# Kernel tuning notes

Hardware: AMD Instinct MI355X
Metric: run time of the kernel (lower is better)

The kernel has to match this reference:

```python
import jax, jax.numpy as jnp
import numpy as np

N_DRUGS = 4096
W_DIM = 512
N_SUB = 10
N_EDGES = 131072


def setup_inputs() -> dict:
    key = jax.random.key(0)
    k1, k2, k3, k4 = jax.random.split(key, 4)
    z_drug = jax.random.normal(k1, (N_DRUGS, W_DIM), dtype=jnp.float32)
    # glorot-ish init for weights
    global_weight = jax.random.normal(k2, (W_DIM, W_DIM), dtype=jnp.float32) * (2.0 / (2 * W_DIM)) ** 0.5
    local_diag = jax.random.normal(k3, (N_SUB, W_DIM), dtype=jnp.float32) * (2.0 / (W_DIM + 1)) ** 0.5
    batch_edges = jax.random.randint(k4, (2, N_EDGES), 0, N_DRUGS, dtype=jnp.int64)
    return {
        "z_drug": z_drug,
        "global_weight": global_weight,
        "local_diag": local_diag,
        "batch_edges": batch_edges,
        "edge_sub_type_idx": 2,
    }


def reference(z_drug, global_weight, local_diag, batch_edges, edge_sub_type_idx):
    # edge_type == 'drug_drug': z1 = z2 = z_drug
    row_embed = z_drug[batch_edges[0]]            # [B, D]
    col_embed = z_drug[batch_edges[1]]            # [B, D]
    d = local_diag[edge_sub_type_idx]             # [D] diagonal of local weight matrix
    # row @ diag(d) @ W @ diag(d) == ((row * d) @ W) * d
    p = ((row_embed * d) @ global_weight) * d     # [B, D]
    # diagonal(p @ col^T) == rowwise dot product
    score = jnp.sum(p * col_embed, axis=-1)       # [B]
    return jax.nn.sigmoid(score)
```

## Files before the change

kernel.cpp:

```cpp
#include <hip/hip_runtime.h>
#include <cstdint>

#define ND 4096
#define D  512

typedef __bf16 bf16x8 __attribute__((ext_vector_type(8)));
typedef float floatx4 __attribute__((ext_vector_type(4)));
typedef unsigned short ushort8 __attribute__((ext_vector_type(8)));

__device__ __forceinline__ float bf2f(unsigned short b) {
    return __uint_as_float(((unsigned int)b) << 16);
}
__device__ __forceinline__ unsigned short f2bf(float f) {
    unsigned int u = __float_as_uint(f);
    u += 0x7fffu + ((u >> 16) & 1u);
    return (unsigned short)(u >> 16);
}
__device__ __forceinline__ float lo16(unsigned int u) { return __uint_as_float(u << 16); }
__device__ __forceinline__ float hi16(unsigned int u) { return __uint_as_float(u & 0xffff0000u); }

__device__ __forceinline__ void gll16(const void* g, void* l) {
    __builtin_amdgcn_global_load_lds((const __attribute__((address_space(1))) unsigned int*)g,
                                     (__attribute__((address_space(3))) unsigned int*)l,
                                     16, 0, 0);
}

union U8B8 { ushort8 u; bf16x8 b; };

__device__ __forceinline__ int2 detect_flags(const unsigned short* z, const int* ed) {
    int lane = threadIdx.x & 63;
    unsigned short u = z[lane];
    int e = (u >> 7) & 0xFF;
    unsigned long long b0 = __ballot(e >= 96 && e <= 160);
    unsigned long long b1 = __ballot(ed[2 * lane + 1] == 0);
    int2 f;
    f.x = (__popcll(b0) >= 56) ? 1 : 0;
    f.y = (__popcll(b1) >= 56) ? 1 : 0;
    return f;
}

__global__ __launch_bounds__(256) void prep_kernel(const void* __restrict__ Wv,
                                                   const void* __restrict__ ldv,
                                                   const int* __restrict__ sub,
                                                   unsigned short* __restrict__ Mt,
                                                   unsigned short* __restrict__ zb,
                                                   const void* __restrict__ z,
                                                   const int* __restrict__ ed) {
    __shared__ float xp[64][65];
    int2 f = detect_flags((const unsigned short*)z, ed);
    int bf = f.x;

    if (blockIdx.x >= 64) {
        if (bf) return;
        int idx = (int)(blockIdx.x - 64) * 256 + threadIdx.x;
        const float* zf = (const float*)z;
#pragma unroll
        for (int it = 0; it < 4; it++) {
            int base = (it * 65536 + idx) * 8;
            float4 f0 = *(const float4*)(zf + base);
            float4 f1 = *(const float4*)(zf + base + 4);
            union { ushort8 u; uint4 v; } cv;
            cv.u[0] = f2bf(f0.x); cv.u[1] = f2bf(f0.y);
            cv.u[2] = f2bf(f0.z); cv.u[3] = f2bf(f0.w);
            cv.u[4] = f2bf(f1.x); cv.u[5] = f2bf(f1.y);
            cv.u[6] = f2bf(f1.z); cv.u[7] = f2bf(f1.w);
            *(uint4*)(zb + base) = cv.v;
        }
        return;
    }

    int su = sub[0];
    if ((unsigned)su > 9u) su = 2;
    int k0 = (blockIdx.x & 7) * 64, n0 = (blockIdx.x >> 3) * 64;
    int j = threadIdx.x & 63, w = threadIdx.x >> 6;
#pragma unroll
    for (int r = 0; r < 16; r++) {
        int k = k0 + w * 16 + r;
        float v = bf ? bf2f(((const unsigned short*)Wv)[k * D + n0 + j])
                     : ((const float*)Wv)[k * D + n0 + j];
        xp[w * 16 + r][j] = v;
    }
    __syncthreads();
    int k = k0 + j;
    float dk = bf ? bf2f(((const unsigned short*)ldv)[su * D + k])
                  : ((const float*)ldv)[su * D + k];
#pragma unroll
    for (int r = 0; r < 16; r++) {
        int n = n0 + w * 16 + r;
        float dn = bf ? bf2f(((const unsigned short*)ldv)[su * D + n])
                      : ((const float*)ldv)[su * D + n];
        Mt[n * D + k] = f2bf(xp[j][w * 16 + r] * dk * dn);
    }
}

__global__ __launch_bounds__(256) void gemm_kernel(const void* __restrict__ z,
                                                   const unsigned short* __restrict__ zb,
                                                   const unsigned short* __restrict__ Mt,
                                                   unsigned short* __restrict__ Y,
                                                   const int* __restrict__ ed) {
    __shared__ __bf16 As[2][8 * 512];
    __shared__ __bf16 Bs[2][8 * 512];
    int2 f = detect_flags((const unsigned short*)z, ed);
    const unsigned short* A = f.x ? (const unsigned short*)z : zb;

    int tid = threadIdx.x;
    int w = tid >> 6, lane = tid & 63;
    int rl = lane & 15, quad = lane >> 4;
    int bx = blockIdx.x;
    int xcd = bx & 7, idx = bx >> 3;
    int tm = (xcd * 8 + (idx & 7)) * 64;
    int tn = (idx >> 3) * 64;
    int wm = (w >> 1) * 32, wn = (w & 1) * 32;

    const unsigned short* Ap = A + (tm + lane) * D;
    const unsigned short* Bp = Mt + (tn + lane) * D;

    floatx4 acc[2][2] = {};

    auto stage = [&](int buf, int kk) {
#pragma unroll
        for (int t = 0; t < 2; t++) {
            int kb = w * 2 + t;
            gll16(Bp + kk + kb * 8, &Bs[buf][kb * 512]);
            gll16(Ap + kk + kb * 8, &As[buf][kb * 512]);
        }
    };
    auto compute = [&](int buf) {
#pragma unroll
        for (int kc = 0; kc < 64; kc += 32) {
            int kb0 = kc >> 3;
            bf16x8 a0 = *(const bf16x8*)(&As[buf][(kb0 + quad) * 512 + (wm + rl) * 8]);
            bf16x8 a1 = *(const bf16x8*)(&As[buf][(kb0 + quad) * 512 + (wm + 16 + rl) * 8]);
            bf16x8 b0 = *(const bf16x8*)(&Bs[buf][(kb0 + quad) * 512 + (wn + rl) * 8]);
            bf16x8 b1 = *(const bf16x8*)(&Bs[buf][(kb0 + quad) * 512 + (wn + 16 + rl) * 8]);
            acc[0][0] = __builtin_amdgcn_mfma_f32_16x16x32_bf16(a0, b0, acc[0][0], 0, 0, 0);
            acc[0][1] = __builtin_amdgcn_mfma_f32_16x16x32_bf16(a0, b1, acc[0][1], 0, 0, 0);
            acc[1][0] = __builtin_amdgcn_mfma_f32_16x16x32_bf16(a1, b0, acc[1][0], 0, 0, 0);
            acc[1][1] = __builtin_amdgcn_mfma_f32_16x16x32_bf16(a1, b1, acc[1][1], 0, 0, 0);
        }
    };

    stage(0, 0);
    __syncthreads();
#pragma unroll
    for (int kt = 1; kt < 8; kt++) {
        int cur = (kt - 1) & 1;
        stage(cur ^ 1, kt * 64);
        compute(cur);
        __syncthreads();
    }
    compute(1);

#pragma unroll
    for (int j = 0; j < 2; j++) {
        int col = tn + wn + j * 16 + rl;
#pragma unroll
        for (int i = 0; i < 2; i++) {
            int rbase = tm + wm + i * 16 + quad * 4;
#pragma unroll
            for (int r = 0; r < 4; r++)
                Y[(rbase + r) * D + col] = f2bf(acc[i][j][r]);
        }
    }
}

template <bool BF, bool I64>
__device__ void edge_slice_body(const unsigned short* __restrict__ Y,
                                const void* __restrict__ z,
                                const int* __restrict__ ed,
                                float* __restrict__ partial, int E) {
    int slice = blockIdx.x & 7;
    int egrp  = blockIdx.x >> 3;
    int lane = threadIdx.x & 63;
    int w = threadIdx.x >> 6;
    int sub8 = lane >> 3;
    int l = lane & 7;
    int col = slice * 64 + l * 8;
    int e0 = egrp * 256 + w * 8 + sub8;

    if (egrp * 256 + 255 < E) {
        int r[8], c[8];
#pragma unroll
        for (int i = 0; i < 8; i++) {
            int e = e0 + i * 32;
            if constexpr (I64) { r[i] = ed[2 * e] & (ND - 1); c[i] = ed[2 * (E + e)] & (ND - 1); }
            else               { r[i] = ed[e] & (ND - 1);     c[i] = ed[E + e] & (ND - 1); }
        }
        float s[8];
#pragma unroll
        for (int i = 0; i < 8; i++) {
            uint4 yu = *(const uint4*)(Y + r[i] * D + col);
            if constexpr (BF) {
                uint4 zu = *(const uint4*)((const unsigned short*)z + c[i] * D + col);
                s[i]  = lo16(yu.x) * lo16(zu.x) + hi16(yu.x) * hi16(zu.x);
                s[i] += lo16(yu.y) * lo16(zu.y) + hi16(yu.y) * hi16(zu.y);
                s[i] += lo16(yu.z) * lo16(zu.z) + hi16(yu.z) * hi16(zu.z);
                s[i] += lo16(yu.w) * lo16(zu.w) + hi16(yu.w) * hi16(zu.w);
            } else {
                const float* zf = (const float*)z + c[i] * D + col;
                float4 f0 = *(const float4*)zf;
                float4 f1 = *(const float4*)(zf + 4);
                s[i]  = lo16(yu.x) * f0.x + hi16(yu.x) * f0.y;
                s[i] += lo16(yu.y) * f0.z + hi16(yu.y) * f0.w;
                s[i] += lo16(yu.z) * f1.x + hi16(yu.z) * f1.y;
                s[i] += lo16(yu.w) * f1.z + hi16(yu.w) * f1.w;
            }
        }
#pragma unroll
        for (int i = 0; i < 8; i++) {
            s[i] += __shfl_xor(s[i], 1, 64);
            s[i] += __shfl_xor(s[i], 2, 64);
            s[i] += __shfl_xor(s[i], 4, 64);
            if (l == 0)
                partial[slice * E + e0 + i * 32] = s[i];
        }
    } else {
#pragma unroll
        for (int i = 0; i < 8; i++) {
            int e = e0 + i * 32;
            if (e >= E) continue;
            int r, c;
            if constexpr (I64) { r = ed[2 * e]; c = ed[2 * (E + e)]; }
            else               { r = ed[e];     c = ed[E + e]; }
            r &= ND - 1; c &= ND - 1;
            uint4 yu = *(const uint4*)(Y + r * D + col);
            float s;
            if constexpr (BF) {
                uint4 zu = *(const uint4*)((const unsigned short*)z + c * D + col);
                s  = lo16(yu.x) * lo16(zu.x) + hi16(yu.x) * hi16(zu.x);
                s += lo16(yu.y) * lo16(zu.y) + hi16(yu.y) * hi16(zu.y);
                s += lo16(yu.z) * lo16(zu.z) + hi16(yu.z) * hi16(zu.z);
                s += lo16(yu.w) * lo16(zu.w) + hi16(yu.w) * hi16(zu.w);
            } else {
                const float* zf = (const float*)z + c * D + col;
                float4 f0 = *(const float4*)zf;
                float4 f1 = *(const float4*)(zf + 4);
                s  = lo16(yu.x) * f0.x + hi16(yu.x) * f0.y;
                s += lo16(yu.y) * f0.z + hi16(yu.y) * f0.w;
                s += lo16(yu.z) * f1.x + hi16(yu.z) * f1.y;
                s += lo16(yu.w) * f1.z + hi16(yu.w) * f1.w;
            }
            s += __shfl_xor(s, 1, 64);
            s += __shfl_xor(s, 2, 64);
            s += __shfl_xor(s, 4, 64);
            if (l == 0)
                partial[slice * E + e] = s;
        }
    }
}

__global__ __launch_bounds__(256) void edge_slice(const unsigned short* __restrict__ Y,
                                                  const void* __restrict__ z,
                                                  const int* __restrict__ ed,
                                                  float* __restrict__ partial, int E) {
    int2 f = detect_flags((const unsigned short*)z, ed);
    if (f.x) { if (f.y) edge_slice_body<true, true >(Y, z, ed, partial, E);
               else     edge_slice_body<true, false>(Y, z, ed, partial, E); }
    else     { if (f.y) edge_slice_body<false, true >(Y, z, ed, partial, E);
               else     edge_slice_body<false, false>(Y, z, ed, partial, E); }
}

__global__ __launch_bounds__(256) void finish_kernel(const float* __restrict__ partial,
                                                     const unsigned short* __restrict__ zdet,
                                                     const int* __restrict__ eddet,
                                                     void* __restrict__ out, int E) {
    int2 f = detect_flags(zdet, eddet);
    int e = blockIdx.x * 256 + threadIdx.x;
    if (e >= E) return;
    float t = 0.f;
#pragma unroll
    for (int s = 0; s < 8; s++)
        t += partial[s * E + e];
    if (!(t > -1e30f && t < 1e30f)) t = 0.0f;
    float sig = 1.0f / (1.0f + __expf(-t));
    if (f.x) ((unsigned short*)out)[e] = f2bf(sig);
    else     ((float*)out)[e] = sig;
}

extern "C" void kernel_launch(void* const* d_in, const int* in_sizes, int n_in,
                              void* d_out, int out_size, void* d_ws, size_t ws_size,
                              hipStream_t stream) {
    const void* z     = d_in[0];
    const void* W     = d_in[1];
    const void* ldiag = d_in[2];
    const int* edges  = (const int*)d_in[3];
    const int* sub    = (const int*)d_in[4];
    int E = out_size;

    char* ws = (char*)d_ws;
    unsigned short* Y  = (unsigned short*)ws;
    unsigned short* Mt = (unsigned short*)(ws + 4194304);
    float* partial     = (float*)(ws + 4194304 + 524288);
    unsigned short* zb = (unsigned short*)(ws + 4194304 + 524288 + 4194304);

    prep_kernel<<<320, 256, 0, stream>>>(W, ldiag, sub, Mt, zb, z, edges);
    gemm_kernel<<<512, 256, 0, stream>>>(z, zb, Mt, Y, edges);
    int sblocks = ((E + 255) / 256) * 8;
    edge_slice<<<sblocks, 256, 0, stream>>>(Y, z, edges, partial, E);
    finish_kernel<<<(E + 255) / 256, 256, 0, stream>>>(partial, (const unsigned short*)z,
                                                       edges, d_out, E);
}
```

Before: 107.2 us.

## Fuse four kernels into one cooperative persistent kernel with grid syncs

```diff
diff --git a/kernel.cpp b/kernel.cpp
--- a/kernel.cpp
+++ b/kernel.cpp
@@ -1,5 +1,8 @@
 #include <hip/hip_runtime.h>
+#include <hip/hip_cooperative_groups.h>
 #include <cstdint>
+
+namespace cg = cooperative_groups;
 
 #define ND 4096
 #define D  512
@@ -24,8 +27,6 @@
                                      (__attribute__((address_space(3))) unsigned int*)l,
                                      16, 0, 0);
 }
-
-union U8B8 { ushort8 u; bf16x8 b; };
 
 __device__ __forceinline__ int2 detect_flags(const unsigned short* z, const int* ed) {
     int lane = threadIdx.x & 63;
@@ -39,40 +40,16 @@
     return f;
 }
 
-__global__ __launch_bounds__(256) void prep_kernel(const void* __restrict__ Wv,
-                                                   const void* __restrict__ ldv,
-                                                   const int* __restrict__ sub,
-                                                   unsigned short* __restrict__ Mt,
-                                                   unsigned short* __restrict__ zb,
-                                                   const void* __restrict__ z,
-                                                   const int* __restrict__ ed) {
-    __shared__ float xp[64][65];
-    int2 f = detect_flags((const unsigned short*)z, ed);
-    int bf = f.x;
-
-    if (blockIdx.x >= 64) {
-        if (bf) return;
-        int idx = (int)(blockIdx.x - 64) * 256 + threadIdx.x;
-        const float* zf = (const float*)z;
-#pragma unroll
-        for (int it = 0; it < 4; it++) {
-            int base = (it * 65536 + idx) * 8;
-            float4 f0 = *(const float4*)(zf + base);
-            float4 f1 = *(const float4*)(zf + base + 4);
-            union { ushort8 u; uint4 v; } cv;
-            cv.u[0] = f2bf(f0.x); cv.u[1] = f2bf(f0.y);
-            cv.u[2] = f2bf(f0.z); cv.u[3] = f2bf(f0.w);
-            cv.u[4] = f2bf(f1.x); cv.u[5] = f2bf(f1.y);
-            cv.u[6] = f2bf(f1.z); cv.u[7] = f2bf(f1.w);
-            *(uint4*)(zb + base) = cv.v;
-        }
-        return;
-    }
-
+
+__device__ __forceinline__ void mt_body(const void* __restrict__ Wv,
+                                        const void* __restrict__ ldv,
+                                        const int* __restrict__ sub,
+                                        unsigned short* __restrict__ Mt,
+                                        int bf, int bid, int tid, float (*xp)[65]) {
     int su = sub[0];
     if ((unsigned)su > 9u) su = 2;
-    int k0 = (blockIdx.x & 7) * 64, n0 = (blockIdx.x >> 3) * 64;
-    int j = threadIdx.x & 63, w = threadIdx.x >> 6;
+    int k0 = (bid & 7) * 64, n0 = (bid >> 3) * 64;
+    int j = tid & 63, w = tid >> 6;
 #pragma unroll
     for (int r = 0; r < 16; r++) {
         int k = k0 + w * 16 + r;
@@ -93,46 +70,52 @@
     }
 }
 
-__global__ __launch_bounds__(256) void gemm_kernel(const void* __restrict__ z,
-                                                   const unsigned short* __restrict__ zb,
-                                                   const unsigned short* __restrict__ Mt,
-                                                   unsigned short* __restrict__ Y,
-                                                   const int* __restrict__ ed) {
-    __shared__ __bf16 As[2][8 * 512];
-    __shared__ __bf16 Bs[2][8 * 512];
-    int2 f = detect_flags((const unsigned short*)z, ed);
-    const unsigned short* A = f.x ? (const unsigned short*)z : zb;
-
-    int tid = threadIdx.x;
+__device__ __forceinline__ void zconv_body(const float* __restrict__ zf,
+                                           unsigned short* __restrict__ zb,
+                                           int v0, int stride) {
+    for (int v = v0; v < (ND * D) / 8; v += stride) {
+        int base = v * 8;
+        float4 f0 = *(const float4*)(zf + base);
+        float4 f1 = *(const float4*)(zf + base + 4);
+        union { ushort8 u; uint4 q; } cv;
+        cv.u[0] = f2bf(f0.x); cv.u[1] = f2bf(f0.y);
+        cv.u[2] = f2bf(f0.z); cv.u[3] = f2bf(f0.w);
+        cv.u[4] = f2bf(f1.x); cv.u[5] = f2bf(f1.y);
+        cv.u[6] = f2bf(f1.z); cv.u[7] = f2bf(f1.w);
+        *(uint4*)(zb + base) = cv.q;
+    }
+}
+
+__device__ __forceinline__ void gemm_tile(const unsigned short* __restrict__ A,
+                                          const unsigned short* __restrict__ Mt,
+                                          unsigned short* __restrict__ Y,
+                                          __bf16* As, __bf16* Bs, int bid, int tid) {
     int w = tid >> 6, lane = tid & 63;
     int rl = lane & 15, quad = lane >> 4;
-    int bx = blockIdx.x;
-    int xcd = bx & 7, idx = bx >> 3;
+    int xcd = bid & 7, idx = bid >> 3;
     int tm = (xcd * 8 + (idx & 7)) * 64;
     int tn = (idx >> 3) * 64;
     int wm = (w >> 1) * 32, wn = (w & 1) * 32;
-
     const unsigned short* Ap = A + (tm + lane) * D;
     const unsigned short* Bp = Mt + (tn + lane) * D;
 
     floatx4 acc[2][2] = {};
-
     auto stage = [&](int buf, int kk) {
 #pragma unroll
         for (int t = 0; t < 2; t++) {
             int kb = w * 2 + t;
-            gll16(Bp + kk + kb * 8, &Bs[buf][kb * 512]);
-            gll16(Ap + kk + kb * 8, &As[buf][kb * 512]);
+            gll16(Bp + kk + kb * 8, Bs + buf * 4096 + kb * 512);
+            gll16(Ap + kk + kb * 8, As + buf * 4096 + kb * 512);
         }
     };
     auto compute = [&](int buf) {
 #pragma unroll
         for (int kc = 0; kc < 64; kc += 32) {
             int kb0 = kc >> 3;
-            bf16x8 a0 = *(const bf16x8*)(&As[buf][(kb0 + quad) * 512 + (wm + rl) * 8]);
-            bf16x8 a1 = *(const bf16x8*)(&As[buf][(kb0 + quad) * 512 + (wm + 16 + rl) * 8]);
-            bf16x8 b0 = *(const bf16x8*)(&Bs[buf][(kb0 + quad) * 512 + (wn + rl) * 8]);
-            bf16x8 b1 = *(const bf16x8*)(&Bs[buf][(kb0 + quad) * 512 + (wn + 16 + rl) * 8]);
+            bf16x8 a0 = *(const bf16x8*)(As + buf * 4096 + (kb0 + quad) * 512 + (wm + rl) * 8);
+            bf16x8 a1 = *(const bf16x8*)(As + buf * 4096 + (kb0 + quad) * 512 + (wm + 16 + rl) * 8);
+            bf16x8 b0 = *(const bf16x8*)(Bs + buf * 4096 + (kb0 + quad) * 512 + (wn + rl) * 8);
+            bf16x8 b1 = *(const bf16x8*)(Bs + buf * 4096 + (kb0 + quad) * 512 + (wn + 16 + rl) * 8);
             acc[0][0] = __builtin_amdgcn_mfma_f32_16x16x32_bf16(a0, b0, acc[0][0], 0, 0, 0);
             acc[0][1] = __builtin_amdgcn_mfma_f32_16x16x32_bf16(a0, b1, acc[0][1], 0, 0, 0);
             acc[1][0] = __builtin_amdgcn_mfma_f32_16x16x32_bf16(a1, b0, acc[1][0], 0, 0, 0);
@@ -165,14 +148,11 @@
 }
 
 template <bool BF, bool I64>
-__device__ void edge_slice_body(const unsigned short* __restrict__ Y,
-                                const void* __restrict__ z,
-                                const int* __restrict__ ed,
-                                float* __restrict__ partial, int E) {
-    int slice = blockIdx.x & 7;
-    int egrp  = blockIdx.x >> 3;
-    int lane = threadIdx.x & 63;
-    int w = threadIdx.x >> 6;
+__device__ __forceinline__ void edge_grp(const unsigned short* __restrict__ Y,
+                                         const void* __restrict__ z,
+                                         const int* __restrict__ ed,
+                                         float* __restrict__ partial, int E,
+                                         int slice, int egrp, int lane, int w) {
     int sub8 = lane >> 3;
     int l = lane & 7;
     int col = slice * 64 + l * 8;
@@ -249,15 +229,100 @@
     }
 }
 
+
+union SMem {
+    float xp[64][65];
+    struct { __bf16 A[2 * 4096]; __bf16 B[2 * 4096]; } g;
+};
+
+__global__ __launch_bounds__(256, 2) void fused_kernel(
+        const void* __restrict__ z, const void* __restrict__ Wv,
+        const void* __restrict__ ldv, const int* __restrict__ ed,
+        const int* __restrict__ sub, unsigned short* __restrict__ Mt,
+        unsigned short* __restrict__ zb, unsigned short* __restrict__ Y,
+        float* __restrict__ partial, void* __restrict__ out, int E) {
+    __shared__ SMem sm;
+    cg::grid_group grid = cg::this_grid();
+    int2 f = detect_flags((const unsigned short*)z, ed);
+    int tid = threadIdx.x, bid = blockIdx.x;
+
+    if (bid < 64)      mt_body(Wv, ldv, sub, Mt, f.x, bid, tid, sm.xp);
+    else if (!f.x)     zconv_body((const float*)z, zb, (bid - 64) * 256 + tid, 448 * 256);
+    grid.sync();
+
+    {
+        const unsigned short* A = f.x ? (const unsigned short*)z : zb;
+        gemm_tile(A, Mt, Y, sm.g.A, sm.g.B, bid, tid);
+    }
+    grid.sync();
+
+    {
+        int lane = tid & 63, w = tid >> 6;
+        int ngrp = (E + 255) >> 8;
+        int slice = bid & 7;
+        if (f.x) {
+            if (f.y) { for (int g0 = bid >> 3; g0 < ngrp; g0 += 64)
+                           edge_grp<true, true >(Y, z, ed, partial, E, slice, g0, lane, w); }
+            else     { for (int g0 = bid >> 3; g0 < ngrp; g0 += 64)
+                           edge_grp<true, false>(Y, z, ed, partial, E, slice, g0, lane, w); }
+        } else {
+            if (f.y) { for (int g0 = bid >> 3; g0 < ngrp; g0 += 64)
+                           edge_grp<false, true >(Y, z, ed, partial, E, slice, g0, lane, w); }
+            else     { for (int g0 = bid >> 3; g0 < ngrp; g0 += 64)
+                           edge_grp<false, false>(Y, z, ed, partial, E, slice, g0, lane, w); }
+        }
+    }
+    grid.sync();
+
+    for (int e = bid * 256 + tid; e < E; e += 512 * 256) {
+        float t = 0.f;
+#pragma unroll
+        for (int s = 0; s < 8; s++)
+            t += partial[s * E + e];
+        if (!(t > -1e30f && t < 1e30f)) t = 0.0f;
+        float sig = 1.0f / (1.0f + __expf(-t));
+        if (f.x) ((unsigned short*)out)[e] = f2bf(sig);
+        else     ((float*)out)[e] = sig;
+    }
+}
+
+
+__global__ __launch_bounds__(256) void prep_kernel(const void* __restrict__ Wv,
+                                                   const void* __restrict__ ldv,
+                                                   const int* __restrict__ sub,
+                                                   unsigned short* __restrict__ Mt,
+                                                   unsigned short* __restrict__ zb,
+                                                   const void* __restrict__ z,
+                                                   const int* __restrict__ ed) {
+    __shared__ float xp[64][65];
+    int2 f = detect_flags((const unsigned short*)z, ed);
+    if (blockIdx.x < 64) mt_body(Wv, ldv, sub, Mt, f.x, blockIdx.x, threadIdx.x, xp);
+    else if (!f.x)
+        zconv_body((const float*)z, zb, (int)(blockIdx.x - 64) * 256 + threadIdx.x, 256 * 256);
+}
+
+__global__ __launch_bounds__(256) void gemm_kernel(const void* __restrict__ z,
+                                                   const unsigned short* __restrict__ zb,
+                                                   const unsigned short* __restrict__ Mt,
+                                                   unsigned short* __restrict__ Y,
+                                                   const int* __restrict__ ed) {
+    __shared__ SMem sm;
+    int2 f = detect_flags((const unsigned short*)z, ed);
+    const unsigned short* A = f.x ? (const unsigned short*)z : zb;
+    gemm_tile(A, Mt, Y, sm.g.A, sm.g.B, blockIdx.x, threadIdx.x);
+}
+
 __global__ __launch_bounds__(256) void edge_slice(const unsigned short* __restrict__ Y,
                                                   const void* __restrict__ z,
                                                   const int* __restrict__ ed,
                                                   float* __restrict__ partial, int E) {
     int2 f = detect_flags((const unsigned short*)z, ed);
-    if (f.x) { if (f.y) edge_slice_body<true, true >(Y, z, ed, partial, E);
-               else     edge_slice_body<true, false>(Y, z, ed, partial, E); }
-    else     { if (f.y) edge_slice_body<false, true >(Y, z, ed, partial, E);
-               else     edge_slice_body<false, false>(Y, z, ed, partial, E); }
+    int lane = threadIdx.x & 63, w = threadIdx.x >> 6;
+    int slice = blockIdx.x & 7, egrp = blockIdx.x >> 3;
+    if (f.x) { if (f.y) edge_grp<true, true >(Y, z, ed, partial, E, slice, egrp, lane, w);
+               else     edge_grp<true, false>(Y, z, ed, partial, E, slice, egrp, lane, w); }
+    else     { if (f.y) edge_grp<false, true >(Y, z, ed, partial, E, slice, egrp, lane, w);
+               else     edge_grp<false, false>(Y, z, ed, partial, E, slice, egrp, lane, w); }
 }
 
 __global__ __launch_bounds__(256) void finish_kernel(const float* __restrict__ partial,
@@ -276,6 +341,7 @@
     if (f.x) ((unsigned short*)out)[e] = f2bf(sig);
     else     ((float*)out)[e] = sig;
 }
+
 
 extern "C" void kernel_launch(void* const* d_in, const int* in_sizes, int n_in,
                               void* d_out, int out_size, void* d_ws, size_t ws_size,
@@ -293,10 +359,19 @@
     float* partial     = (float*)(ws + 4194304 + 524288);
     unsigned short* zb = (unsigned short*)(ws + 4194304 + 524288 + 4194304);
 
-    prep_kernel<<<320, 256, 0, stream>>>(W, ldiag, sub, Mt, zb, z, edges);
-    gemm_kernel<<<512, 256, 0, stream>>>(z, zb, Mt, Y, edges);
-    int sblocks = ((E + 255) / 256) * 8;
-    edge_slice<<<sblocks, 256, 0, stream>>>(Y, z, edges, partial, E);
-    finish_kernel<<<(E + 255) / 256, 256, 0, stream>>>(partial, (const unsigned short*)z,
-                                                       edges, d_out, E);
-}
+    void* outp = d_out;
+    void* args[] = {(void*)&z, (void*)&W, (void*)&ldiag, (void*)&edges, (void*)&sub,
+                    (void*)&Mt, (void*)&zb, (void*)&Y, (void*)&partial, (void*)&outp,
+                    (void*)&E};
+    hipError_t err = hipLaunchCooperativeKernel((const void*)fused_kernel,
+                                                dim3(512), dim3(256), args, 0, stream);
+    if (err != hipSuccess) {
+        (void)hipGetLastError();
+        prep_kernel<<<320, 256, 0, stream>>>(W, ldiag, sub, Mt, zb, z, edges);
+        gemm_kernel<<<512, 256, 0, stream>>>(z, zb, Mt, Y, edges);
+        int sblocks = ((E + 255) / 256) * 8;
+        edge_slice<<<sblocks, 256, 0, stream>>>(Y, z, edges, partial, E);
+        finish_kernel<<<(E + 255) / 256, 256, 0, stream>>>(partial, (const unsigned short*)z,
+                                                           edges, d_out, E);
+    }
+}
```

New measurement: 307.4 us. 2.87x slower.
